# Kernel optimization log

Hardware: AMD Instinct MI355X
Metric: run time of the kernel (lower is better)

## Reference

```python
import jax, jax.numpy as jnp
import numpy as np

B_SZ, CH, H, W = 32, 256, 28, 28
D_INNER, D_STATE, D_CONV, DT_RANK, DEPTH = 512, 16, 4, 16, 2


def setup_inputs() -> dict:
    key = jax.random.key(0)
    ks = jax.random.split(key, 10)
    s = 0.02
    A = jnp.broadcast_to(jnp.arange(1, D_STATE + 1, dtype=jnp.float32), (DEPTH, D_INNER, D_STATE))
    return {
        "bbox_feats": jax.random.normal(ks[0], (B_SZ, CH, H, W), jnp.float32),
        "norm_w": jnp.ones((DEPTH, CH), jnp.float32),
        "norm_b": jnp.zeros((DEPTH, CH), jnp.float32),
        "in_proj_w": jax.random.normal(ks[1], (DEPTH, 2 * D_INNER, CH), jnp.float32) * s,
        "conv_w": jax.random.normal(ks[2], (DEPTH, D_INNER, D_CONV), jnp.float32) * 0.1,
        "conv_b": jnp.zeros((DEPTH, D_INNER), jnp.float32),
        "x_proj_w": jax.random.normal(ks[3], (DEPTH, DT_RANK + 2 * D_STATE, D_INNER), jnp.float32) * s,
        "dt_proj_w": jax.random.normal(ks[4], (DEPTH, D_INNER, DT_RANK), jnp.float32) * 0.1,
        "dt_proj_b": jax.random.normal(ks[5], (DEPTH, D_INNER), jnp.float32) * 0.1,
        "A_log": jnp.log(A),
        "D_param": jnp.ones((DEPTH, D_INNER), jnp.float32),
        "out_proj_w": jax.random.normal(ks[6], (DEPTH, CH, D_INNER), jnp.float32) * s,
    }


def _layernorm(x, w, b, eps=1e-5):
    mu = jnp.mean(x, axis=-1, keepdims=True)
    var = jnp.mean(jnp.square(x - mu), axis=-1, keepdims=True)
    return (x - mu) * jax.lax.rsqrt(var + eps) * w + b


def _mamba(x, in_w, cw, cb, xp_w, dtp_w, dtp_b, A_log, Dp, out_w):
    # x: [B, L, d_model]
    B, L, _ = x.shape
    xz = jnp.einsum('bld,ed->ble', x, in_w)          # [B, L, 2*d_inner]
    xi, z = jnp.split(xz, 2, axis=-1)                # each [B, L, d_inner]
    # depthwise causal conv1d (kernel D_CONV, left pad D_CONV-1)
    xpad = jnp.pad(xi, ((0, 0), (D_CONV - 1, 0), (0, 0)))
    xc = cb
    for k in range(D_CONV):
        xc = xc + xpad[:, k:k + L, :] * cw[:, k]
    xc = jax.nn.silu(xc)                             # [B, L, d_inner]
    x_dbl = jnp.einsum('bld,ed->ble', xc, xp_w)      # [B, L, dt_rank+2*d_state]
    dt_r = x_dbl[..., :DT_RANK]
    Bm = x_dbl[..., DT_RANK:DT_RANK + D_STATE]
    Cm = x_dbl[..., DT_RANK + D_STATE:]
    dt = jax.nn.softplus(jnp.einsum('blr,dr->bld', dt_r, dtp_w) + dtp_b)  # [B, L, d_inner]
    A = -jnp.exp(A_log)                              # [d_inner, d_state]

    def step(h, inp):
        dt_t, B_t, C_t, x_t = inp                    # [B,d_inner],[B,d_state],[B,d_state],[B,d_inner]
        dA = jnp.exp(dt_t[:, :, None] * A)           # [B, d_inner, d_state]
        h = h * dA + dt_t[:, :, None] * B_t[:, None, :] * x_t[:, :, None]
        y = jnp.einsum('bds,bs->bd', h, C_t)
        return h, y

    h0 = jnp.zeros((B, D_INNER, D_STATE), x.dtype)
    inputs = (jnp.swapaxes(dt, 0, 1), jnp.swapaxes(Bm, 0, 1),
              jnp.swapaxes(Cm, 0, 1), jnp.swapaxes(xc, 0, 1))
    _, ys = jax.lax.scan(step, h0, inputs)
    y = jnp.swapaxes(ys, 0, 1) + xc * Dp             # [B, L, d_inner]
    y = y * jax.nn.silu(z)
    return jnp.einsum('bld,ed->ble', y, out_w)       # [B, L, d_model]


def reference(bbox_feats, norm_w, norm_b, in_proj_w, conv_w, conv_b,
              x_proj_w, dt_proj_w, dt_proj_b, A_log, D_param, out_proj_w):
    B, C, h, w = bbox_feats.shape
    x = bbox_feats
    for i in range(DEPTH):
        xf = jnp.swapaxes(x.reshape(B, C, h * w), -1, -2)   # [B, L, C]
        xn = _layernorm(xf, norm_w[i], norm_b[i])
        ym = _mamba(xn, in_proj_w[i], conv_w[i], conv_b[i], x_proj_w[i],
                    dt_proj_w[i], dt_proj_b[i], A_log[i], D_param[i], out_proj_w[i])
        x = jnp.swapaxes(ym, -1, -2).reshape(B, C, h, w)
    return x
```

## Files before the change

kernel.cpp:

```cpp
#include <hip/hip_runtime.h>
#include <cstdint>
#include <cstddef>

#define BSZ  32
#define CHN  256
#define LSEQ 784
#define DI   512
#define NCH  8
#define LC   98

typedef unsigned short u16;
typedef short s16x8 __attribute__((ext_vector_type(8)));
typedef float f32x4 __attribute__((ext_vector_type(4)));

__device__ __forceinline__ float b2f(u16 u) {
  union { unsigned int i; float f; } v; v.i = ((unsigned int)u) << 16; return v.f;
}
__device__ __forceinline__ u16 f2b(float f) {
  union { float f; unsigned int i; } v; v.f = f;
  unsigned int x = v.i;
  return (u16)((x + 0x7FFFu + ((x >> 16) & 1u)) >> 16);
}

__global__ void k_flag(const unsigned* __restrict__ nwraw, int* __restrict__ flag) {
  if (threadIdx.x == 0 && blockIdx.x == 0) {
    flag[0] = (nwraw[0] == 0x3F803F80u) ? 1 : 0;
    flag[1] = 1;
  }
}

__global__ __launch_bounds__(256) void k_canon(const void* __restrict__ src,
                                               u16* __restrict__ dst, int n,
                                               const int* __restrict__ flag) {
  int i = blockIdx.x * 2048 + threadIdx.x;
  if (flag[0]) {
    const u16* s = (const u16*)src;
#pragma unroll
    for (int q = 0; q < 8; q++) {
      int j = i + q * 256;
      if (j < n) dst[j] = s[j];
    }
  } else {
    const float* s = (const float*)src;
#pragma unroll
    for (int q = 0; q < 8; q++) {
      int j = i + q * 256;
      if (j < n) dst[j] = f2b(s[j]);
    }
  }
}

__global__ __launch_bounds__(256) void k_norm(const void* __restrict__ xv,
                                              int b0,
                                              const int* __restrict__ flag,
                                              const u16* __restrict__ nw,
                                              const u16* __restrict__ nb,
                                              u16* __restrict__ xn) {
  bool isbf = flag[0] != 0;
  int b  = blockIdx.y;
  int gb = b0 + b;
  int l0 = blockIdx.x * 64;
  int tx = threadIdx.x & 63;
  int ty = threadIdx.x >> 6;
  int l  = l0 + tx;
  bool valid = l < LSEQ;
  const u16*   xb16 = (const u16*)xv   + (size_t)gb * CHN * LSEQ;
  const float* xb32 = (const float*)xv + (size_t)gb * CHN * LSEQ;
  float s = 0.f, sq = 0.f;
  for (int c = ty; c < CHN; c += 4) {
    size_t idx = (size_t)c * LSEQ + l;
    float v = 0.f;
    if (valid) v = isbf ? b2f(xb16[idx]) : xb32[idx];
    s += v; sq += v * v;
  }
  __shared__ float rs[4][64], rq[4][64], smu[64], srs[64];
  rs[ty][tx] = s; rq[ty][tx] = sq;
  __syncthreads();
  if (ty == 0) {
    float ss = rs[0][tx] + rs[1][tx] + rs[2][tx] + rs[3][tx];
    float qq = rq[0][tx] + rq[1][tx] + rq[2][tx] + rq[3][tx];
    float mu  = ss * (1.f / CHN);
    float var = qq * (1.f / CHN) - mu * mu;
    smu[tx] = mu;
    srs[tx] = rsqrtf(var + 1e-5f);
  }
  __syncthreads();
  if (valid) {
    float mu = smu[tx], rstd = srs[tx];
    u16* xnb = xn + (size_t)b * CHN * LSEQ;
    for (int c = ty; c < CHN; c += 4) {
      size_t idx = (size_t)c * LSEQ + l;
      float v = isbf ? b2f(xb16[idx]) : xb32[idx];
      xnb[idx] = f2b((v - mu) * rstd * b2f(nw[c]) + b2f(nb[c]));
    }
  }
}

template <int MODE>
__global__ __launch_bounds__(256) void k_gmm(const u16* __restrict__ A,
                                             const u16* __restrict__ W,
                                             float* __restrict__ C0,
                                             u16* __restrict__ Cb0,
                                             u16* __restrict__ Cb1,
                                             void* __restrict__ Dout,
                                             const int* __restrict__ flag,
                                             int b0, int K, int Ntot) {
  __shared__ unsigned ldsA[128 * 20];
  __shared__ unsigned ldsW[64 * 20];
  int tid = threadIdx.x;
  int m0 = blockIdx.x * 128;
  int n0 = blockIdx.y * 64;
  int b  = blockIdx.z;
  int w    = tid >> 6;
  int l15  = tid & 15;
  int quad = (tid >> 4) & 3;
  int kp = tid & 15;
  int mo = tid >> 4;
  int wn = tid >> 2;
  int wc = tid & 3;

  const u16* Ab = A + (size_t)b * K * LSEQ;

  f32x4 acc[8];
#pragma unroll
  for (int i = 0; i < 8; i++)
#pragma unroll
    for (int r = 0; r < 4; r++) acc[i][r] = 0.f;

  for (int k0 = 0; k0 < K; k0 += 32) {
    __syncthreads();
    {
      int mg = m0 + mo * 8;
      unsigned lo[4] = {0u, 0u, 0u, 0u}, hi[4] = {0u, 0u, 0u, 0u};
      if (mg < LSEQ) {
        int4 r0 = *(const int4*)(Ab + (size_t)(k0 + 2 * kp) * LSEQ + mg);
        int4 r1 = *(const int4*)(Ab + (size_t)(k0 + 2 * kp + 1) * LSEQ + mg);
        lo[0] = (unsigned)r0.x; lo[1] = (unsigned)r0.y;
        lo[2] = (unsigned)r0.z; lo[3] = (unsigned)r0.w;
        hi[0] = (unsigned)r1.x; hi[1] = (unsigned)r1.y;
        hi[2] = (unsigned)r1.z; hi[3] = (unsigned)r1.w;
      }
#pragma unroll
      for (int j = 0; j < 8; j++) {
        unsigned lov = (lo[j >> 1] >> ((j & 1) * 16)) & 0xFFFFu;
        unsigned hiv = (hi[j >> 1] >> ((j & 1) * 16)) & 0xFFFFu;
        ldsA[(mo * 8 + j) * 20 + kp] = lov | (hiv << 16);
      }
    }
    {
      int ng = n0 + wn;
      int4 r = make_int4(0, 0, 0, 0);
      if (ng < Ntot) r = *(const int4*)(W + (size_t)ng * K + k0 + wc * 8);
      *(int4*)(ldsW + wn * 20 + wc * 4) = r;
    }
    __syncthreads();
    s16x8 bf = *(const s16x8*)(ldsW + ((w * 16 + l15) * 20 + quad * 4));
#pragma unroll
    for (int mi = 0; mi < 8; mi++) {
      s16x8 af = *(const s16x8*)(ldsA + ((mi * 16 + l15) * 20 + quad * 4));
      acc[mi] = __builtin_amdgcn_mfma_f32_16x16x32_bf16(af, bf, acc[mi], 0, 0, 0);
    }
  }

  int n_g = n0 + w * 16 + l15;
  if (n_g >= Ntot) return;
#pragma unroll
  for (int mi = 0; mi < 8; mi++) {
    int mb = m0 + mi * 16;
    if (mb >= LSEQ) break;
    int m = mb + quad * 4;
    float v0 = acc[mi][0], v1 = acc[mi][1], v2 = acc[mi][2], v3 = acc[mi][3];
    if constexpr (MODE == 0) {
      float* crow = C0 + ((size_t)b * Ntot + n_g) * LSEQ + m;
      *(float4*)crow = make_float4(v0, v1, v2, v3);
    } else if constexpr (MODE == 3) {
      size_t off = ((size_t)(b0 + b) * Ntot + n_g) * LSEQ + m;
      if (flag[0]) {
        u16* crow = (u16*)Dout + off;
        ((unsigned*)crow)[0] = (unsigned)f2b(v0) | ((unsigned)f2b(v1) << 16);
        ((unsigned*)crow)[1] = (unsigned)f2b(v2) | ((unsigned)f2b(v3) << 16);
      } else {
        float* crow = (float*)Dout + off;
        *(float4*)crow = make_float4(v0, v1, v2, v3);
      }
    } else {
      u16* crow;
      if constexpr (MODE == 1) {
        crow = (n_g < DI) ? (Cb0 + ((size_t)b * DI + n_g) * LSEQ + m)
                          : (Cb1 + ((size_t)b * DI + (n_g - DI)) * LSEQ + m);
      } else {
        crow = Cb0 + ((size_t)b * Ntot + n_g) * LSEQ + m;
      }
      ((unsigned*)crow)[0] = (unsigned)f2b(v0) | ((unsigned)f2b(v1) << 16);
      ((unsigned*)crow)[1] = (unsigned)f2b(v2) | ((unsigned)f2b(v3) << 16);
    }
  }
}

__global__ __launch_bounds__(256) void k_conv(const u16* __restrict__ xi,
                                              const u16* __restrict__ cw,
                                              const u16* __restrict__ cb,
                                              u16* __restrict__ xc) {
  int b = blockIdx.z, e = blockIdx.y;
  int l = blockIdx.x * 256 + threadIdx.x;
  if (l >= LSEQ) return;
  const u16* xr = xi + ((size_t)b * DI + e) * LSEQ;
  float acc = b2f(cb[e]);
#pragma unroll
  for (int k = 0; k < 4; k++) {
    int li = l - 3 + k;
    if (li >= 0) acc += b2f(xr[li]) * b2f(cw[e * 4 + k]);
  }
  acc = acc / (1.f + __expf(-acc));
  xc[((size_t)b * DI + e) * LSEQ + l] = f2b(acc);
}

__global__ __launch_bounds__(256) void k_trbc(const float* __restrict__ xd,
                                              float* __restrict__ BC) {
  int b = blockIdx.y;
  int l = blockIdx.x * 256 + threadIdx.x;
  if (l >= LSEQ) return;
  float* dst = BC + ((size_t)b * LSEQ + l) * 32;
#pragma unroll
  for (int j = 0; j < 32; j++)
    dst[j] = xd[((size_t)b * 48 + 16 + j) * LSEQ + l];
}

__device__ __forceinline__ float softplus_f(float x) {
  float t = __expf(x);
  return (x > 20.f) ? x : __logf(1.f + t);
}

__global__ __launch_bounds__(256) void k_dtp(const float* __restrict__ xd,
                                             const u16* __restrict__ dtw,
                                             const u16* __restrict__ dtbv,
                                             u16* __restrict__ dtp) {
  __shared__ float Ls[16][64];
  int b  = blockIdx.y;
  int l0 = blockIdx.x * 64;
  int tid = threadIdx.x;
  const float* xb = xd + (size_t)b * 48 * LSEQ;
  for (int idx = tid; idx < 16 * 64; idx += 256) {
    int r = idx >> 6, lo = idx & 63;
    int l = l0 + lo;
    Ls[r][lo] = (l < LSEQ) ? xb[(size_t)r * LSEQ + l] : 0.f;
  }
  __syncthreads();
  int tx = tid & 63, ty = tid >> 6;
  int l = l0 + tx;
  if (l >= LSEQ) return;
  u16* drow = dtp + (size_t)b * DI * LSEQ + l;
  for (int eg = 0; eg < 128; eg++) {
    int e = ty * 128 + eg;
    float acc = b2f(dtbv[e]);
#pragma unroll
    for (int r = 0; r < 16; r++) acc += Ls[r][tx] * b2f(dtw[e * 16 + r]);
    drow[(size_t)e * LSEQ] = f2b(softplus_f(acc));
  }
}

__global__ __launch_bounds__(256) void k_scanA(const u16* __restrict__ dtp,
                                               const float* __restrict__ BC,
                                               const u16* __restrict__ xc,
                                               const u16* __restrict__ A_log,
                                               float* __restrict__ P,
                                               float* __restrict__ hloc) {
  __shared__ unsigned xs[256 * 13];
  __shared__ unsigned ds[256 * 13];
  int tid = threadIdx.x;
  int b = blockIdx.x >> 4;
  int e = ((blockIdx.x & 15) << 5) + (tid & 31);
  int chunk = tid >> 5;
  float a[16];
  bool pow_ok = true;
#pragma unroll
  for (int n = 0; n < 16; n++) {
    a[n] = -__expf(b2f(A_log[e * 16 + n]));
    pow_ok = pow_ok && (fabsf(a[n] + (float)(n + 1)) < 0.02f * (n + 1));
  }
  float h[16];
#pragma unroll
  for (int n = 0; n < 16; n++) h[n] = 0.f;
  float S = 0.f;
  const float* bcb = BC + (size_t)b * LSEQ * 32;
  const u16* xrow = xc  + ((size_t)b * DI + e) * LSEQ + chunk * LC;
  const u16* drow = dtp + ((size_t)b * DI + e) * LSEQ + chunk * LC;
  unsigned* myx = xs + tid * 13;
  unsigned* myd = ds + tid * 13;
  int lbase = chunk * LC;
#pragma unroll
  for (int t = 0; t < 4; t++) {
    int off = t * 24;
    int nd  = (t < 3) ? 12 : 13;
    {
      const unsigned* gx = (const unsigned*)(xrow + off);
      for (int j = 0; j < nd; j++) myx[j] = gx[j];
      const unsigned* gd = (const unsigned*)(drow + off);
      for (int j = 0; j < nd; j++) myd[j] = gd[j];
    }
    int T = nd * 2;
    for (int s = 0; s < T; s++) {
      int l = lbase + off + s;
      unsigned wd = myd[s >> 1];
      unsigned wx = myx[s >> 1];
      float d  = b2f((s & 1) ? (u16)(wd >> 16) : (u16)(wd & 0xFFFFu));
      float xt = b2f((s & 1) ? (u16)(wx >> 16) : (u16)(wx & 0xFFFFu));
      S += d;
      const float4* bp = (const float4*)(bcb + (size_t)l * 32);
      float4 B0 = bp[0], B1 = bp[1], B2 = bp[2], B3 = bp[3];
      float Bv[16] = {B0.x,B0.y,B0.z,B0.w, B1.x,B1.y,B1.z,B1.w,
                      B2.x,B2.y,B2.z,B2.w, B3.x,B3.y,B3.z,B3.w};
      float dx = d * xt;
      if (pow_ok) {
        float w = __expf(-d);
        float da = 1.f;
#pragma unroll
        for (int n = 0; n < 16; n++) {
          da *= w;
          h[n] = h[n] * da + dx * Bv[n];
        }
      } else {
#pragma unroll
        for (int n = 0; n < 16; n++) {
          float da = __expf(d * a[n]);
          h[n] = h[n] * da + dx * Bv[n];
        }
      }
    }
  }
  size_t base = (((size_t)b * DI + e) * NCH + chunk) * 16;
  float4* Pp = (float4*)(P + base);
  float4* Hp = (float4*)(hloc + base);
  if (pow_ok) {
    float pw = __expf(-S);
    float pa = 1.f;
#pragma unroll
    for (int q = 0; q < 4; q++) {
      float p0 = pa * pw, p1 = p0 * pw, p2 = p1 * pw, p3 = p2 * pw;
      Pp[q] = make_float4(p0, p1, p2, p3);
      pa = p3;
      Hp[q] = make_float4(h[q*4], h[q*4+1], h[q*4+2], h[q*4+3]);
    }
  } else {
#pragma unroll
    for (int q = 0; q < 4; q++) {
      Pp[q] = make_float4(__expf(a[q*4+0] * S), __expf(a[q*4+1] * S),
                          __expf(a[q*4+2] * S), __expf(a[q*4+3] * S));
      Hp[q] = make_float4(h[q*4], h[q*4+1], h[q*4+2], h[q*4+3]);
    }
  }
}

__global__ __launch_bounds__(256) void k_comb(const float* __restrict__ P,
                                              float* hloc) {
  int idx = blockIdx.x * 256 + threadIdx.x;
  int n  = idx & 15;
  int be = idx >> 4;
  size_t base = (size_t)be * (NCH * 16) + n;
  float h = 0.f;
#pragma unroll
  for (int c = 0; c < NCH; c++) {
    size_t o = base + (size_t)c * 16;
    float hl = hloc[o];
    float pp = P[o];
    hloc[o] = h;
    h = hl + pp * h;
  }
}

__global__ __launch_bounds__(256) void k_scanC(const u16* __restrict__ dtp,
                                               const float* __restrict__ BC,
                                               const u16* __restrict__ zp,
                                               const u16* __restrict__ A_log,
                                               const u16* __restrict__ Dp,
                                               const float* __restrict__ hinit,
                                               u16* xcy) {
  __shared__ unsigned xs[256 * 13];
  __shared__ unsigned zs[256 * 13];
  __shared__ unsigned ds[256 * 13];
  int tid = threadIdx.x;
  int b = blockIdx.x >> 4;
  int e = ((blockIdx.x & 15) << 5) + (tid & 31);
  int chunk = tid >> 5;
  float a[16];
  bool pow_ok = true;
#pragma unroll
  for (int n = 0; n < 16; n++) {
    a[n] = -__expf(b2f(A_log[e * 16 + n]));
    pow_ok = pow_ok && (fabsf(a[n] + (float)(n + 1)) < 0.02f * (n + 1));
  }
  float h[16];
  {
    size_t base = (((size_t)b * DI + e) * NCH + chunk) * 16;
    const float4* Hp = (const float4*)(hinit + base);
#pragma unroll
    for (int q = 0; q < 4; q++) {
      float4 v = Hp[q];
      h[q*4] = v.x; h[q*4+1] = v.y; h[q*4+2] = v.z; h[q*4+3] = v.w;
    }
  }
  float dpar = b2f(Dp[e]);
  const float* bcb = BC + (size_t)b * LSEQ * 32;
  u16* xrow = xcy + ((size_t)b * DI + e) * LSEQ + chunk * LC;
  const u16* zrow = zp  + ((size_t)b * DI + e) * LSEQ + chunk * LC;
  const u16* drow = dtp + ((size_t)b * DI + e) * LSEQ + chunk * LC;
  unsigned* myx = xs + tid * 13;
  unsigned* myz = zs + tid * 13;
  unsigned* myd = ds + tid * 13;
  int lbase = chunk * LC;
  u16 ylo = 0;
#pragma unroll
  for (int t = 0; t < 4; t++) {
    int off = t * 24;
    int nd  = (t < 3) ? 12 : 13;
    {
      const unsigned* gx = (const unsigned*)(xrow + off);
      for (int j = 0; j < nd; j++) myx[j] = gx[j];
      const unsigned* gz = (const unsigned*)(zrow + off);
      for (int j = 0; j < nd; j++) myz[j] = gz[j];
      const unsigned* gd = (const unsigned*)(drow + off);
      for (int j = 0; j < nd; j++) myd[j] = gd[j];
    }
    int T = nd * 2;
    for (int s = 0; s < T; s++) {
      int l = lbase + off + s;
      unsigned wd = myd[s >> 1];
      unsigned wx = myx[s >> 1];
      unsigned wz = myz[s >> 1];
      float d  = b2f((s & 1) ? (u16)(wd >> 16) : (u16)(wd & 0xFFFFu));
      float xt = b2f((s & 1) ? (u16)(wx >> 16) : (u16)(wx & 0xFFFFu));
      float z  = b2f((s & 1) ? (u16)(wz >> 16) : (u16)(wz & 0xFFFFu));
      const float4* bp = (const float4*)(bcb + (size_t)l * 32);
      float4 B0 = bp[0], B1 = bp[1], B2 = bp[2], B3 = bp[3];
      float4 C0 = bp[4], C1 = bp[5], C2 = bp[6], C3 = bp[7];
      float Bv[16] = {B0.x,B0.y,B0.z,B0.w, B1.x,B1.y,B1.z,B1.w,
                      B2.x,B2.y,B2.z,B2.w, B3.x,B3.y,B3.z,B3.w};
      float Cv[16] = {C0.x,C0.y,C0.z,C0.w, C1.x,C1.y,C1.z,C1.w,
                      C2.x,C2.y,C2.z,C2.w, C3.x,C3.y,C3.z,C3.w};
      float dx = d * xt;
      float yacc = 0.f;
      if (pow_ok) {
        float w = __expf(-d);
        float da = 1.f;
#pragma unroll
        for (int n = 0; n < 16; n++) {
          da *= w;
          h[n] = h[n] * da + dx * Bv[n];
          yacc += h[n] * Cv[n];
        }
      } else {
#pragma unroll
        for (int n = 0; n < 16; n++) {
          float da = __expf(d * a[n]);
          h[n] = h[n] * da + dx * Bv[n];
          yacc += h[n] * Cv[n];
        }
      }
      float yy = yacc + xt * dpar;
      float sg = 1.f / (1.f + __expf(-z));
      u16 yb = f2b(yy * (z * sg));
      if (s & 1)
        myx[s >> 1] = (unsigned)ylo | ((unsigned)yb << 16);
      else
        ylo = yb;
    }
    {
      unsigned* gy = (unsigned*)(xrow + off);
      for (int j = 0; j < nd; j++) gy[j] = myx[j];
    }
  }
}

extern "C" void kernel_launch(void* const* d_in, const int* in_sizes, int n_in,
                              void* d_out, int out_size, void* d_ws, size_t ws_size,
                              hipStream_t stream) {
  u16* ws = (u16*)d_ws;

  u16* c_nw  = ws;
  u16* c_nb  = ws + 512;
  u16* c_inw = ws + 1024;
  u16* c_cw  = ws + 525312;
  u16* c_cb  = ws + 529408;
  u16* c_xpw = ws + 530432;
  u16* c_dtw = ws + 579584;
  u16* c_dtb = ws + 595968;
  u16* c_al  = ws + 596992;
  u16* c_dp  = ws + 613376;
  u16* c_ow  = ws + 614400;
  int* flag  = (int*)(ws + 876544);
  const size_t WREG = 876552;

  k_flag<<<1, 64, 0, stream>>>((const unsigned*)d_in[1], flag);
  {
    const void* srcs[11] = {d_in[1], d_in[2], d_in[3], d_in[4], d_in[5], d_in[6],
                            d_in[7], d_in[8], d_in[9], d_in[10], d_in[11]};
    u16* dsts[11] = {c_nw, c_nb, c_inw, c_cw, c_cb, c_xpw,
                     c_dtw, c_dtb, c_al, c_dp, c_ow};
    int ns[11] = {512, 512, 524288, 4096, 1024, 49152,
                  16384, 1024, 16384, 1024, 262144};
    for (int k = 0; k < 11; k++)
      k_canon<<<(ns[k] + 2047) / 2048, 256, 0, stream>>>(srcs[k], dsts[k], ns[k], flag);
  }

  size_t fixed_bytes = WREG * 2;
  size_t per_batch   = 4ull * DI * LSEQ * 2;
  int Bg = 1;
  for (int g = 32; g >= 1; g >>= 1) {
    if (ws_size >= fixed_bytes + (size_t)g * per_batch) { Bg = g; break; }
  }

  size_t plane = (size_t)Bg * DI * LSEQ;
  u16*   pb = ws + WREG;
  u16*   xi = pb;
  float* xd = (float*)pb;
  float* bc = xd + (size_t)Bg * 48 * LSEQ;
  float* Pb = bc + (size_t)Bg * LSEQ * 32;
  float* hl = Pb + (size_t)Bg * DI * NCH * 16;
  u16*   zp = pb + plane;
  u16*   xc = pb + 2 * plane;
  u16*   dtx1 = pb + 3 * plane;
  u16*   dtp = dtx1;
  u16*   x1  = dtx1;
  u16*   xn = xc;

  for (int b0 = 0; b0 < BSZ; b0 += Bg) {
    for (int i = 0; i < 2; i++) {
      if (i == 0)
        k_norm<<<dim3(13, Bg), 256, 0, stream>>>(
            d_in[0], b0, flag, c_nw, c_nb, xn);
      else
        k_norm<<<dim3(13, Bg), 256, 0, stream>>>(
            (const void*)x1, 0, flag + 1, c_nw + CHN, c_nb + CHN, xn);
      k_gmm<1><<<dim3(7, 16, Bg), 256, 0, stream>>>(
          xn, c_inw + (size_t)i * 1024 * CHN, nullptr, xi, zp,
          nullptr, nullptr, 0, CHN, 1024);
      k_conv<<<dim3(4, 512, Bg), 256, 0, stream>>>(
          xi, c_cw + i * DI * 4, c_cb + i * DI, xc);
      k_gmm<0><<<dim3(7, 1, Bg), 256, 0, stream>>>(
          xc, c_xpw + (size_t)i * 48 * DI, xd, nullptr, nullptr,
          nullptr, nullptr, 0, DI, 48);
      k_trbc<<<dim3(4, Bg), 256, 0, stream>>>(xd, bc);
      k_dtp<<<dim3(13, Bg), 256, 0, stream>>>(
          xd, c_dtw + i * DI * 16, c_dtb + i * DI, dtp);
      k_scanA<<<Bg * 16, 256, 0, stream>>>(
          dtp, bc, xc, c_al + i * DI * 16, Pb, hl);
      k_comb<<<Bg * 32, 256, 0, stream>>>(Pb, hl);
      k_scanC<<<Bg * 16, 256, 0, stream>>>(
          dtp, bc, zp, c_al + i * DI * 16, c_dp + i * DI, hl, xc);
      if (i == 0)
        k_gmm<2><<<dim3(7, 4, Bg), 256, 0, stream>>>(
            xc, c_ow, nullptr, x1, nullptr,
            nullptr, nullptr, 0, DI, CHN);
      else
        k_gmm<3><<<dim3(7, 4, Bg), 256, 0, stream>>>(
            xc, c_ow + (size_t)CHN * DI, nullptr, nullptr, nullptr,
            d_out, flag, b0, DI, CHN);
    }
  }
}
```

Before: 938.8 us.

## Split scan into 16 chunks and store per-chunk dt sums instead of decay products

```diff
diff --git a/kernel.cpp b/kernel.cpp
--- a/kernel.cpp
+++ b/kernel.cpp
@@ -6,8 +6,7 @@
 #define CHN  256
 #define LSEQ 784
 #define DI   512
-#define NCH  8
-#define LC   98
+#define NCH  16
 
 typedef unsigned short u16;
 typedef short s16x8 __attribute__((ext_vector_type(8)));
@@ -263,14 +262,15 @@
                                                const float* __restrict__ BC,
                                                const u16* __restrict__ xc,
                                                const u16* __restrict__ A_log,
-                                               float* __restrict__ P,
+                                               float* __restrict__ Sb,
                                                float* __restrict__ hloc) {
   __shared__ unsigned xs[256 * 13];
   __shared__ unsigned ds[256 * 13];
   int tid = threadIdx.x;
-  int b = blockIdx.x >> 4;
-  int e = ((blockIdx.x & 15) << 5) + (tid & 31);
-  int chunk = tid >> 5;
+  int b = blockIdx.x >> 5;
+  int r = blockIdx.x & 31;
+  int e     = ((r >> 1) << 5) + (tid & 31);
+  int chunk = ((r & 1) << 3) + (tid >> 5);
   float a[16];
   bool pow_ok = true;
 #pragma unroll
@@ -282,16 +282,16 @@
 #pragma unroll
   for (int n = 0; n < 16; n++) h[n] = 0.f;
   float S = 0.f;
+  int lbase = chunk * 50;
   const float* bcb = BC + (size_t)b * LSEQ * 32;
-  const u16* xrow = xc  + ((size_t)b * DI + e) * LSEQ + chunk * LC;
-  const u16* drow = dtp + ((size_t)b * DI + e) * LSEQ + chunk * LC;
+  const u16* xrow = xc  + ((size_t)b * DI + e) * LSEQ + lbase;
+  const u16* drow = dtp + ((size_t)b * DI + e) * LSEQ + lbase;
   unsigned* myx = xs + tid * 13;
   unsigned* myd = ds + tid * 13;
-  int lbase = chunk * LC;
-#pragma unroll
-  for (int t = 0; t < 4; t++) {
-    int off = t * 24;
-    int nd  = (t < 3) ? 12 : 13;
+#pragma unroll
+  for (int t = 0; t < 2; t++) {
+    int off = t * 26;
+    int nd  = (t == 0) ? 13 : ((chunk == 15) ? 4 : 12);
     {
       const unsigned* gx = (const unsigned*)(xrow + off);
       for (int j = 0; j < nd; j++) myx[j] = gx[j];
@@ -328,43 +328,32 @@
       }
     }
   }
+  Sb[((size_t)b * DI + e) * NCH + chunk] = S;
   size_t base = (((size_t)b * DI + e) * NCH + chunk) * 16;
-  float4* Pp = (float4*)(P + base);
   float4* Hp = (float4*)(hloc + base);
-  if (pow_ok) {
-    float pw = __expf(-S);
-    float pa = 1.f;
-#pragma unroll
-    for (int q = 0; q < 4; q++) {
-      float p0 = pa * pw, p1 = p0 * pw, p2 = p1 * pw, p3 = p2 * pw;
-      Pp[q] = make_float4(p0, p1, p2, p3);
-      pa = p3;
-      Hp[q] = make_float4(h[q*4], h[q*4+1], h[q*4+2], h[q*4+3]);
-    }
-  } else {
-#pragma unroll
-    for (int q = 0; q < 4; q++) {
-      Pp[q] = make_float4(__expf(a[q*4+0] * S), __expf(a[q*4+1] * S),
-                          __expf(a[q*4+2] * S), __expf(a[q*4+3] * S));
-      Hp[q] = make_float4(h[q*4], h[q*4+1], h[q*4+2], h[q*4+3]);
-    }
-  }
-}
-
-__global__ __launch_bounds__(256) void k_comb(const float* __restrict__ P,
+#pragma unroll
+  for (int q = 0; q < 4; q++)
+    Hp[q] = make_float4(h[q*4], h[q*4+1], h[q*4+2], h[q*4+3]);
+}
+
+__global__ __launch_bounds__(256) void k_comb(const u16* __restrict__ A_log,
+                                              const float* __restrict__ Sb,
                                               float* hloc) {
   int idx = blockIdx.x * 256 + threadIdx.x;
   int n  = idx & 15;
   int be = idx >> 4;
-  size_t base = (size_t)be * (NCH * 16) + n;
+  int e  = be & (DI - 1);
+  float an = -__expf(b2f(A_log[e * 16 + n]));
+  size_t hbase = (size_t)be * (NCH * 16) + n;
+  size_t sbase = (size_t)be * NCH;
   float h = 0.f;
 #pragma unroll
   for (int c = 0; c < NCH; c++) {
-    size_t o = base + (size_t)c * 16;
+    size_t o = hbase + (size_t)c * 16;
     float hl = hloc[o];
-    float pp = P[o];
+    float p  = __expf(an * Sb[sbase + c]);
     hloc[o] = h;
-    h = hl + pp * h;
+    h = hl + p * h;
   }
 }
 
@@ -379,9 +368,10 @@
   __shared__ unsigned zs[256 * 13];
   __shared__ unsigned ds[256 * 13];
   int tid = threadIdx.x;
-  int b = blockIdx.x >> 4;
-  int e = ((blockIdx.x & 15) << 5) + (tid & 31);
-  int chunk = tid >> 5;
+  int b = blockIdx.x >> 5;
+  int r = blockIdx.x & 31;
+  int e     = ((r >> 1) << 5) + (tid & 31);
+  int chunk = ((r & 1) << 3) + (tid >> 5);
   float a[16];
   bool pow_ok = true;
 #pragma unroll
@@ -400,19 +390,19 @@
     }
   }
   float dpar = b2f(Dp[e]);
+  int lbase = chunk * 50;
   const float* bcb = BC + (size_t)b * LSEQ * 32;
-  u16* xrow = xcy + ((size_t)b * DI + e) * LSEQ + chunk * LC;
-  const u16* zrow = zp  + ((size_t)b * DI + e) * LSEQ + chunk * LC;
-  const u16* drow = dtp + ((size_t)b * DI + e) * LSEQ + chunk * LC;
+  u16* xrow = xcy + ((size_t)b * DI + e) * LSEQ + lbase;
+  const u16* zrow = zp  + ((size_t)b * DI + e) * LSEQ + lbase;
+  const u16* drow = dtp + ((size_t)b * DI + e) * LSEQ + lbase;
   unsigned* myx = xs + tid * 13;
   unsigned* myz = zs + tid * 13;
   unsigned* myd = ds + tid * 13;
-  int lbase = chunk * LC;
   u16 ylo = 0;
 #pragma unroll
-  for (int t = 0; t < 4; t++) {
-    int off = t * 24;
-    int nd  = (t < 3) ? 12 : 13;
+  for (int t = 0; t < 2; t++) {
+    int off = t * 26;
+    int nd  = (t == 0) ? 13 : ((chunk == 15) ? 4 : 12);
     {
       const unsigned* gx = (const unsigned*)(xrow + off);
       for (int j = 0; j < nd; j++) myx[j] = gx[j];
@@ -512,10 +502,11 @@
   size_t plane = (size_t)Bg * DI * LSEQ;
   u16*   pb = ws + WREG;
   u16*   xi = pb;
-  float* xd = (float*)pb;
-  float* bc = xd + (size_t)Bg * 48 * LSEQ;
-  float* Pb = bc + (size_t)Bg * LSEQ * 32;
-  float* hl = Pb + (size_t)Bg * DI * NCH * 16;
+  float* fb = (float*)pb;
+  float* bc = fb;
+  float* xd = bc + (size_t)Bg * LSEQ * 32;
+  float* Sb = xd;
+  float* hl = Sb + (size_t)Bg * DI * NCH;
   u16*   zp = pb + plane;
   u16*   xc = pb + 2 * plane;
   u16*   dtx1 = pb + 3 * plane;
@@ -542,10 +533,10 @@
       k_trbc<<<dim3(4, Bg), 256, 0, stream>>>(xd, bc);
       k_dtp<<<dim3(13, Bg), 256, 0, stream>>>(
           xd, c_dtw + i * DI * 16, c_dtb + i * DI, dtp);
-      k_scanA<<<Bg * 16, 256, 0, stream>>>(
-          dtp, bc, xc, c_al + i * DI * 16, Pb, hl);
-      k_comb<<<Bg * 32, 256, 0, stream>>>(Pb, hl);
-      k_scanC<<<Bg * 16, 256, 0, stream>>>(
+      k_scanA<<<Bg * 32, 256, 0, stream>>>(
+          dtp, bc, xc, c_al + i * DI * 16, Sb, hl);
+      k_comb<<<Bg * 32, 256, 0, stream>>>(c_al + i * DI * 16, Sb, hl);
+      k_scanC<<<Bg * 32, 256, 0, stream>>>(
           dtp, bc, zp, c_al + i * DI * 16, c_dp + i * DI, hl, xc);
       if (i == 0)
         k_gmm<2><<<dim3(7, 4, Bg), 256, 0, stream>>>(
```

After: 907.1 us. 3.4% less time.
